# Performance work log

Hardware: AMD Instinct MI355X
Metric: run time of the kernel (lower is better)

Reference implementation:

```python
import math
import jax, jax.numpy as jnp
import numpy as np

N, L, C_IMG, D, FF, H, NL, V = 2, 1024, 512, 512, 2048, 8, 4, 8000
EPS_ATTN = 1e-6
EPS_LN = 1e-5


def pos_enc(position, channels):
    # position: (N, L, 1) float. channels assumed even here (256 / 512).
    num = channels // 2
    log_inc = math.log(10000.0) / (num - 1)
    inv = jnp.exp(jnp.arange(num, dtype=position.dtype) * -log_inc)
    st = position * inv.reshape(1, 1, -1)  # (N, L, num)
    return jnp.concatenate([jnp.sin(st), jnp.cos(st)], -1)


def layer_norm(x, s, b):
    m = jnp.mean(x, -1, keepdims=True)
    v = jnp.mean((x - m) ** 2, -1, keepdims=True)
    return (x - m) / jnp.sqrt(v + EPS_LN) * s + b


def causal_linear_attention(x, mask, Wq, bq, Wk, bk, Wv, bv, Wo, bo):
    # x: (N, L, D), mask: (N, L, 1)
    n, l, d = x.shape
    q = (x @ Wq + bq).reshape(n, l, H, -1)
    k = (x @ Wk + bk).reshape(n, l, H, -1)
    v = (x @ Wv + bv).reshape(n, l, H, -1)
    Q = jax.nn.elu(q) + 1.0                       # elu feature map
    K = (jax.nn.elu(k) + 1.0) * mask[:, :, :, None]
    K_cum = jnp.cumsum(K, axis=1)                 # (N, L, H, dk)
    Z = 1.0 / (jnp.einsum('nlhd,nlhd->nlh', Q, K_cum) + EPS_ATTN)
    KV = jnp.cumsum(K[..., :, None] * v[..., None, :], axis=1)  # (N, L, H, dk, dv)
    out = jnp.einsum('nlhd,nlhde->nlhe', Q, KV) * Z[..., None]
    return out.reshape(n, l, d) @ Wo + bo


def encoder_layer(x, mask, p):
    (Wq, bq, Wk, bk, Wv, bv, Wo, bo, W1, b1, W2, b2, s1, be1, s2, be2) = p
    x = x + causal_linear_attention(x, mask, Wq, bq, Wk, bk, Wv, bv, Wo, bo)
    x = layer_norm(x, s1, be1)
    y = jax.nn.gelu(x @ W1 + b1, approximate=False) @ W2 + b2
    return layer_norm(x + y, s2, be2)


def setup_inputs() -> dict:
    key = jax.random.key(0)
    ks = iter(jax.random.split(key, 64))

    def p(shape):
        return jax.random.normal(next(ks), shape, dtype=jnp.float32) * 0.02

    x_img = jax.random.normal(next(ks), (N, L, C_IMG), dtype=jnp.float32)
    x_txt = jax.random.randint(next(ks), (N, L), 0, V)
    pos = jnp.broadcast_to(jnp.arange(L, dtype=jnp.float32)[None, :, None], (N, L, 1))
    pos_r = jnp.floor(pos / 32.0)
    pos_c = jnp.mod(pos, 32.0)
    pos_t = pos
    first_half = (jnp.arange(L) < L // 2).astype(jnp.float32)[None, :, None]
    mask_img = jnp.broadcast_to(first_half, (N, L, 1))
    mask_txt = 1.0 - mask_img

    inp = dict(x_img=x_img, x_txt=x_txt, mask_img=mask_img, mask_txt=mask_txt,
               pos_r=pos_r, pos_c=pos_c, pos_t=pos_t,
               W_ei=p((C_IMG, D)), b_ei=jnp.zeros((D,)),
               emb_txt=p((V, D)),
               Wq=p((NL, D, D)), bq=jnp.zeros((NL, D)),
               Wk=p((NL, D, D)), bk=jnp.zeros((NL, D)),
               Wv=p((NL, D, D)), bv=jnp.zeros((NL, D)),
               Wo=p((NL, D, D)), bo=jnp.zeros((NL, D)),
               W1=p((NL, D, FF)), b1=jnp.zeros((NL, FF)),
               W2=p((NL, FF, D)), b2=jnp.zeros((NL, D)),
               ln1_s=jnp.ones((NL, D)), ln1_b=jnp.zeros((NL, D)),
               ln2_s=jnp.ones((NL, D)), ln2_b=jnp.zeros((NL, D)),
               W_pi=p((D, C_IMG)), b_pi=jnp.zeros((C_IMG,)),
               W_pt=p((D, V)), b_pt=jnp.zeros((V,)))
    return inp


def reference(x_img, x_txt, mask_img, mask_txt, pos_r, pos_c, pos_t,
              W_ei, b_ei, emb_txt,
              Wq, bq, Wk, bk, Wv, bv, Wo, bo, W1, b1, W2, b2,
              ln1_s, ln1_b, ln2_s, ln2_b, W_pi, b_pi, W_pt, b_pt):
    x_mask = mask_img + mask_txt  # (N, L, 1)
    # image embedding
    half = D // 2
    x_pos = jnp.concatenate([pos_enc(pos_r, half), pos_enc(pos_c, D - half)], -1)
    x_emb_img = ((x_img @ W_ei + b_ei) + x_pos) * mask_img
    # text embedding
    x_emb_txt = (emb_txt[x_txt] + pos_enc(pos_t, D)) * mask_txt
    x = x_emb_img + x_emb_txt
    for i in range(NL):
        p = (Wq[i], bq[i], Wk[i], bk[i], Wv[i], bv[i], Wo[i], bo[i],
             W1[i], b1[i], W2[i], b2[i], ln1_s[i], ln1_b[i], ln2_s[i], ln2_b[i])
        x = encoder_layer(x, x_mask, p)
    logit_img = x @ W_pi + b_pi
    logit_txt = x @ W_pt + b_pt
    return (logit_img, logit_txt)
```

## Files before the change

kernel.cpp:

```cpp
#include <hip/hip_runtime.h>
#include <hip/hip_bf16.h>
#include <math.h>

#define NB 2
#define LSEQ 1024
#define DM 512
#define FFD 2048
#define NHEAD 8
#define DKH 64
#define NLAYER 4
#define VOCAB 8000
#define NCHUNK 16
#define NROWS (NB * LSEQ)
#define QS 1536
#define NHEADCAT 8512
#define NHEADPAD 8576

#define OP_NONE 0
#define OP_GELU 2
#define OP_PART 4
#define OP_HEAD 5

typedef __attribute__((ext_vector_type(8))) short short8;
typedef __attribute__((ext_vector_type(4))) float f32x4;
typedef __hip_bfloat16 bf16;

__device__ __forceinline__ void cast_tile(
    const float* __restrict__ s, bf16* __restrict__ d, int K, int N,
    int n0, int k0, int tid)
{
    __shared__ float tile[32][33];
    const int r  = tid >> 3;
    const int c4 = (tid & 7) * 4;
    const int n  = n0 + c4;
    float4 v = make_float4(0.f, 0.f, 0.f, 0.f);
    if (n < N)
        v = *(const float4*)(s + (size_t)(k0 + r) * N + n);
    tile[r][c4 + 0] = v.x; tile[r][c4 + 1] = v.y;
    tile[r][c4 + 2] = v.z; tile[r][c4 + 3] = v.w;
    __syncthreads();
    const int nr = tid >> 3;
    const int kc = (tid & 7) * 4;
    bf16 o[4];
    o[0] = __float2bfloat16(tile[kc + 0][nr]);
    o[1] = __float2bfloat16(tile[kc + 1][nr]);
    o[2] = __float2bfloat16(tile[kc + 2][nr]);
    o[3] = __float2bfloat16(tile[kc + 3][nr]);
    *(unsigned long long*)(d + (size_t)(n0 + nr) * K + k0 + kc) =
        *(const unsigned long long*)o;
    __syncthreads();
}

#define CO_QKVO 0
#define CO_W1   4096
#define CO_W2   8192
#define CO_WEI  12288
#define CO_WPI  12544
#define CO_WPT  12800
#define CO_XIMG 16832
#define CO_QKVB 17856
#define CO_HB   17860
#define CO_END  17894

__global__ __launch_bounds__(256) void setup_all(
    const float* __restrict__ Wq, const float* __restrict__ Wk,
    const float* __restrict__ Wv, const float* __restrict__ Wo,
    const float* __restrict__ W1, const float* __restrict__ W2,
    const float* __restrict__ Wei, const float* __restrict__ Wpi,
    const float* __restrict__ Wpt,
    bf16* __restrict__ QKVt, bf16* __restrict__ Wot,
    bf16* __restrict__ W1t, bf16* __restrict__ W2t,
    bf16* __restrict__ Weit, bf16* __restrict__ Whead,
    const float* __restrict__ x_img, bf16* __restrict__ ximgh,
    const float* __restrict__ bq, const float* __restrict__ bk,
    const float* __restrict__ bv, float* __restrict__ qkvB,
    const float* __restrict__ bpi, const float* __restrict__ bpt,
    float* __restrict__ hb)
{
    const int id = blockIdx.x;
    const int tid = threadIdx.x;

    if (id < CO_W1) {
        const int rel = id;
        const int z = rel >> 8, t = rel & 255;
        const int layer = z >> 2, which = z & 3;
        const float* src = (which == 0 ? Wq : which == 1 ? Wk : which == 2 ? Wv : Wo)
                           + (size_t)layer * 262144;
        const int n0 = (t & 15) * 32, k0 = (t >> 4) * 32;
        if (which < 3) {
            const int h = n0 >> 6;
            bf16* dst = QKVt + (size_t)layer * 786432
                      + (size_t)(h * 128 + which * 64) * 512;
            cast_tile(src, dst, 512, 512, n0, k0, tid);
        } else {
            cast_tile(src, Wot + (size_t)layer * 262144, 512, 512, n0, k0, tid);
        }
    } else if (id < CO_W2) {
        const int rel = id - CO_W1;
        const int z = rel >> 10, t = rel & 1023;
        cast_tile(W1 + (size_t)z * 1048576, W1t + (size_t)z * 1048576,
                  512, 2048, (t & 63) * 32, (t >> 6) * 32, tid);
    } else if (id < CO_WEI) {
        const int rel = id - CO_W2;
        const int z = rel >> 10, t = rel & 1023;
        cast_tile(W2 + (size_t)z * 1048576, W2t + (size_t)z * 1048576,
                  2048, 512, (t & 15) * 32, (t >> 4) * 32, tid);
    } else if (id < CO_WPI) {
        const int t = id - CO_WEI;
        cast_tile(Wei, Weit, 512, 512, (t & 15) * 32, (t >> 4) * 32, tid);
    } else if (id < CO_WPT) {
        const int t = id - CO_WPI;
        cast_tile(Wpi, Whead, 512, 512, (t & 15) * 32, (t >> 4) * 32, tid);
    } else if (id < CO_XIMG) {
        const int t = id - CO_WPT;
        cast_tile(Wpt, Whead + 262144, 512, VOCAB,
                  (t % 252) * 32, (t / 252) * 32, tid);
    } else if (id < CO_QKVB) {
        const int i = (id - CO_XIMG) * 256 + tid;
        const float4 v = *(const float4*)(x_img + (size_t)i * 4);
        ximgh[(size_t)i * 4 + 0] = __float2bfloat16(v.x);
        ximgh[(size_t)i * 4 + 1] = __float2bfloat16(v.y);
        ximgh[(size_t)i * 4 + 2] = __float2bfloat16(v.z);
        ximgh[(size_t)i * 4 + 3] = __float2bfloat16(v.w);
    } else if (id < CO_HB) {
        const int z = id - CO_QKVB;
        for (int j = tid; j < QS; j += 256) {
            const int h = j / 192, rem = j - h * 192;
            const int which = rem >> 6, idx = rem & 63;
            const float* bsrc = (which == 0 ? bq : which == 1 ? bk : bv);
            qkvB[z * QS + j] = bsrc[z * DM + h * 64 + idx];
        }
    } else {
        const int j = (id - CO_HB) * 256 + tid;
        if (j < NHEADPAD)
            hb[j] = (j < 512) ? bpi[j] : (j < NHEADCAT ? bpt[j - 512] : 0.f);
    }
}

template<int BM, int BN>
__global__ __launch_bounds__(256) void gemm16(
    const bf16* __restrict__ A, const bf16* __restrict__ Bt,
    const float* __restrict__ bias,
    float* __restrict__ outF, float* __restrict__ outF2,
    bf16* __restrict__ outH,
    int M, int K, int Nout, int op, int kslab)
{
    constexpr int WM = BM / 2, WN = BN / 2, MI = WM / 16, NI = WN / 16;
    constexpr int LA = BM / 64, LB = BN / 64;
    constexpr int NL = LA + LB;
    __shared__ bf16 As[2][BM * 32];
    __shared__ bf16 Bs[2][BN * 32];
    const int tid = threadIdx.x;
    const int lane = tid & 63;
    const int wave = tid >> 6;
    const int wm = (wave >> 1) * WM, wn = (wave & 1) * WN;

    int bxi = blockIdx.x, byi = blockIdx.y;
    if (op == OP_HEAD) {
        const int gx = gridDim.x;
        const int nwg = gx * gridDim.y;
        int flat = byi * gx + bxi;
        const int q = nwg >> 3, r = nwg & 7;
        const int xcd = flat & 7, lid = flat >> 3;
        flat = (xcd < r ? xcd * (q + 1) : r * (q + 1) + (xcd - r) * q) + lid;
        bxi = flat % gx;
        byi = flat / gx;
    }
    const int bm = (op == OP_HEAD ? bxi : blockIdx.y) * BM;
    const int bn = (op == OP_HEAD ? byi : blockIdx.x) * BN;
    const int l16 = lane & 15, quad = lane >> 4;

    const int rA = tid >> 2;
    const int c8 = (tid & 3) << 3;

    f32x4 acc[MI][NI];
    #pragma unroll
    for (int i = 0; i < MI; ++i)
        #pragma unroll
        for (int j = 0; j < NI; ++j) acc[i][j] = (f32x4){0.f, 0.f, 0.f, 0.f};

    const bf16* gA = A  + (size_t)(bm + rA) * K + c8;
    const bf16* gB = Bt + (size_t)(bn + rA) * K + c8;
    const int ldsWaveOff = wave * 1024;

    const int kStart = blockIdx.z * kslab;
    const int kEnd = kStart + kslab;

    auto stage = [&](int buf, int k0) {
        #pragma unroll
        for (int i = 0; i < LA; ++i)
            __builtin_amdgcn_global_load_lds(
                (const __attribute__((address_space(1))) void*)(gA + (size_t)i * 64 * K + k0),
                (__attribute__((address_space(3))) void*)((char*)As[buf] + i * 4096 + ldsWaveOff),
                16, 0, 0);
        #pragma unroll
        for (int i = 0; i < LB; ++i)
            __builtin_amdgcn_global_load_lds(
                (const __attribute__((address_space(1))) void*)(gB + (size_t)i * 64 * K + k0),
                (__attribute__((address_space(3))) void*)((char*)Bs[buf] + i * 4096 + ldsWaveOff),
                16, 0, 0);
    };

    stage(0, kStart);
    int cur = 0;
    for (int k0 = kStart; k0 < kEnd; k0 += 32) {
        const bool hasNext = (k0 + 32 < kEnd);
        if (hasNext) {
            stage(cur ^ 1, k0 + 32);
            asm volatile("s_waitcnt vmcnt(%0)" :: "n"(NL) : "memory");
        } else {
            asm volatile("s_waitcnt vmcnt(0)" ::: "memory");
        }
        __builtin_amdgcn_s_barrier();
        short8 a[MI], b[NI];
        #pragma unroll
        for (int i = 0; i < MI; ++i)
            a[i] = *(const short8*)(As[cur] + (size_t)(wm + i * 16 + l16) * 32 + quad * 8);
        #pragma unroll
        for (int j = 0; j < NI; ++j)
            b[j] = *(const short8*)(Bs[cur] + (size_t)(wn + j * 16 + l16) * 32 + quad * 8);
        #pragma unroll
        for (int i = 0; i < MI; ++i)
            #pragma unroll
            for (int j = 0; j < NI; ++j)
                acc[i][j] = __builtin_amdgcn_mfma_f32_16x16x32_bf16(
                    b[j], a[i], acc[i][j], 0, 0, 0);
        __builtin_amdgcn_s_barrier();
        cur ^= 1;
    }

    if (op == OP_PART) {
        float* dst = outF + (size_t)blockIdx.z * (size_t)M * Nout;
        #pragma unroll
        for (int i = 0; i < MI; ++i) {
            const int row = bm + wm + i * 16 + l16;
            #pragma unroll
            for (int j = 0; j < NI; ++j) {
                const int colb = bn + wn + j * 16 + quad * 4;
                *(f32x4*)(dst + (size_t)row * Nout + colb) = acc[i][j];
            }
        }
        return;
    }
    if (op == OP_HEAD) {
        #pragma unroll
        for (int i = 0; i < MI; ++i) {
            const int row = bm + wm + i * 16 + l16;
            #pragma unroll
            for (int j = 0; j < NI; ++j) {
                const int colb = bn + wn + j * 16 + quad * 4;
                const bool cok = (colb < NHEADCAT);
                if (!cok) continue;
                const float4 bz = *(const float4*)(bias + colb);
                f32x4 v = acc[i][j];
                v[0] += bz.x; v[1] += bz.y; v[2] += bz.z; v[3] += bz.w;
                if (colb < 512)
                    *(f32x4*)(outF + (size_t)row * 512 + colb) = v;
                else
                    *(f32x4*)(outF2 + (size_t)row * VOCAB + (colb - 512)) = v;
            }
        }
        return;
    }

    #pragma unroll
    for (int i = 0; i < MI; ++i) {
        const int row = bm + wm + i * 16 + l16;
        #pragma unroll
        for (int j = 0; j < NI; ++j) {
            const int colb = bn + wn + j * 16 + quad * 4;
            if (colb >= Nout) continue;
            const float4 bz = bias ? *(const float4*)(bias + colb)
                                   : make_float4(0.f, 0.f, 0.f, 0.f);
            float v[4];
            #pragma unroll
            for (int r = 0; r < 4; ++r) {
                v[r] = acc[i][j][r] + ((const float*)&bz)[r];
                if (op == OP_GELU)
                    v[r] = 0.5f * v[r] * (1.f + erff(v[r] * 0.70710678118654752f));
            }
            if (outF)
                *(f32x4*)(outF + (size_t)row * Nout + colb) =
                    (f32x4){v[0], v[1], v[2], v[3]};
            if (outH) {
                bf16 o[4];
                o[0] = __float2bfloat16(v[0]); o[1] = __float2bfloat16(v[1]);
                o[2] = __float2bfloat16(v[2]); o[3] = __float2bfloat16(v[3]);
                *(unsigned long long*)(outH + (size_t)row * Nout + colb) =
                    *(const unsigned long long*)o;
            }
        }
    }
}

__global__ __launch_bounds__(256) void qkv_attn(
    const bf16* __restrict__ A, const bf16* __restrict__ Bt,
    const float* __restrict__ bias,
    float* __restrict__ QKVb, float* __restrict__ S, float* __restrict__ ks)
{
    __shared__ char smem[33792];
    const int c = blockIdx.x, h = blockIdx.y, n = blockIdx.z;
    const int tid = threadIdx.x;
    const int lane = tid & 63;
    const int wave = tid >> 6;
    const int l16 = lane & 15, quad = lane >> 4;
    const int r0 = n * LSEQ + c * 64;
    const int wn = wave * 48;

    const bf16* Bh = Bt + (size_t)(h * 192) * 512;
    const float* bh = bias + h * 192;

    f32x4 acc[4][3];
    #pragma unroll
    for (int i = 0; i < 4; ++i)
        #pragma unroll
        for (int j = 0; j < 3; ++j) acc[i][j] = (f32x4){0.f, 0.f, 0.f, 0.f};

    const bf16* gA = A + (size_t)(r0 + (tid >> 2)) * 512 + ((tid & 3) << 3);
    const int ldsWaveOff = wave * 1024;

    auto stage = [&](int buf, int k0) {
        __builtin_amdgcn_global_load_lds(
            (const __attribute__((address_space(1))) void*)(gA + k0),
            (__attribute__((address_space(3))) void*)(smem + buf * 4096 + ldsWaveOff),
            16, 0, 0);
        #pragma unroll
        for (int p = 0; p < 3; ++p)
            __builtin_amdgcn_global_load_lds(
                (const __attribute__((address_space(1))) void*)(
                    Bh + (size_t)(p * 64 + (tid >> 2)) * 512 + ((tid & 3) << 3) + k0),
                (__attribute__((address_space(3))) void*)(
                    smem + 8192 + buf * 12288 + p * 4096 + ldsWaveOff),
                16, 0, 0);
    };

    stage(0, 0);
    int cur = 0;
    for (int k0 = 0; k0 < 512; k0 += 32) {
        if (k0 + 32 < 512) {
            stage(cur ^ 1, k0 + 32);
            asm volatile("s_waitcnt vmcnt(4)" ::: "memory");
        } else {
            asm volatile("s_waitcnt vmcnt(0)" ::: "memory");
        }
        __builtin_amdgcn_s_barrier();
        const bf16* Asb = (const bf16*)(smem + cur * 4096);
        const bf16* Bsb = (const bf16*)(smem + 8192 + cur * 12288);
        short8 a[4], b[3];
        #pragma unroll
        for (int i = 0; i < 4; ++i)
            a[i] = *(const short8*)(Asb + (i * 16 + l16) * 32 + quad * 8);
        #pragma unroll
        for (int j = 0; j < 3; ++j)
            b[j] = *(const short8*)(Bsb + (wn + j * 16 + l16) * 32 + quad * 8);
        #pragma unroll
        for (int i = 0; i < 4; ++i)
            #pragma unroll
            for (int j = 0; j < 3; ++j)
                acc[i][j] = __builtin_amdgcn_mfma_f32_16x16x32_bf16(
                    b[j], a[i], acc[i][j], 0, 0, 0);
        __builtin_amdgcn_s_barrier();
        cur ^= 1;
    }
    __syncthreads();

    float* sK   = (float*)smem;
    float* sV   = (float*)(smem + 16384);
    float* part = (float*)(smem + 32768);

    #pragma unroll
    for (int i = 0; i < 4; ++i) {
        const int row = i * 16 + l16;
        #pragma unroll
        for (int j = 0; j < 3; ++j) {
            const int colb = wn + j * 16 + quad * 4;
            const float4 bz = *(const float4*)(bh + colb);
            float v[4];
            #pragma unroll
            for (int r = 0; r < 4; ++r) {
                v[r] = acc[i][j][r] + ((const float*)&bz)[r];
                if (colb < 128) v[r] = (v[r] > 0.f) ? v[r] + 1.f : expf(v[r]);
            }
            int gcolb;
            if (colb < 64)       gcolb = h * 64 + colb;
            else if (colb < 128) gcolb = 512 + h * 64 + (colb - 64);
            else                 gcolb = 1024 + h * 64 + (colb - 128);
            *(f32x4*)(QKVb + (size_t)(r0 + row) * QS + gcolb) =
                (f32x4){v[0], v[1], v[2], v[3]};
            if (colb >= 128)
                *(f32x4*)(sV + row * 64 + (colb - 128)) = (f32x4){v[0], v[1], v[2], v[3]};
            else if (colb >= 64)
                *(f32x4*)(sK + row * 64 + (colb - 64))  = (f32x4){v[0], v[1], v[2], v[3]};
        }
    }
    __syncthreads();

    const int e = tid & 63, dq = tid >> 6;
    float s[16] = {};
    for (int l = 0; l < 64; ++l) {
        const float vv = sV[l * 64 + e];
        const float4 k0v = *(const float4*)(sK + l * 64 + dq * 16 + 0);
        const float4 k1v = *(const float4*)(sK + l * 64 + dq * 16 + 4);
        const float4 k2v = *(const float4*)(sK + l * 64 + dq * 16 + 8);
        const float4 k3v = *(const float4*)(sK + l * 64 + dq * 16 + 12);
        s[0]  = fmaf(k0v.x, vv, s[0]);  s[1]  = fmaf(k0v.y, vv, s[1]);
        s[2]  = fmaf(k0v.z, vv, s[2]);  s[3]  = fmaf(k0v.w, vv, s[3]);
        s[4]  = fmaf(k1v.x, vv, s[4]);  s[5]  = fmaf(k1v.y, vv, s[5]);
        s[6]  = fmaf(k1v.z, vv, s[6]);  s[7]  = fmaf(k1v.w, vv, s[7]);
        s[8]  = fmaf(k2v.x, vv, s[8]);  s[9]  = fmaf(k2v.y, vv, s[9]);
        s[10] = fmaf(k2v.z, vv, s[10]); s[11] = fmaf(k2v.w, vv, s[11]);
        s[12] = fmaf(k3v.x, vv, s[12]); s[13] = fmaf(k3v.y, vv, s[13]);
        s[14] = fmaf(k3v.z, vv, s[14]); s[15] = fmaf(k3v.w, vv, s[15]);
    }
    const size_t sb = (((size_t)(n * NHEAD + h)) * NCHUNK + c) * 4096;
    #pragma unroll
    for (int i = 0; i < 16; ++i) S[sb + (size_t)(dq * 16 + i) * 64 + e] = s[i];

    float kp = 0.f;
    #pragma unroll
    for (int i = 0; i < 16; ++i) kp += sK[(dq * 16 + i) * 64 + e];
    part[dq * 64 + e] = kp;
    __syncthreads();
    if (tid < 64)
        ks[(((size_t)(n * NHEAD + h)) * NCHUNK + c) * 64 + tid] =
            part[tid] + part[64 + tid] + part[128 + tid] + part[192 + tid];
}

__global__ __launch_bounds__(256) void embed_k(
    const float* __restrict__ gI, const int* __restrict__ xt,
    const float* __restrict__ emb,
    const float* __restrict__ mi, const float* __restrict__ mt,
    const float* __restrict__ pr, const float* __restrict__ pc,
    const float* __restrict__ pt, float* __restrict__ X, bf16* __restrict__ Xh)
{
    const int row = blockIdx.x;
    const float prv = pr[row], pcv = pc[row], ptv = pt[row];
    const float miv = mi[row], mtv = mt[row];
    const int tok = xt[row];
    const float LOG1E4 = 9.2103403719761836f;
    const float LI127 = LOG1E4 / 127.f;
    const float LI255 = LOG1E4 / 255.f;

    for (int d = threadIdx.x; d < DM; d += 256) {
        float ip;
        if (d < 128)       ip = sinf(prv * expf(-(float)d * LI127));
        else if (d < 256)  ip = cosf(prv * expf(-(float)(d - 128) * LI127));
        else if (d < 384)  ip = sinf(pcv * expf(-(float)(d - 256) * LI127));
        else               ip = cosf(pcv * expf(-(float)(d - 384) * LI127));
        float tp;
        if (d < 256) tp = sinf(ptv * expf(-(float)d * LI255));
        else         tp = cosf(ptv * expf(-(float)(d - 256) * LI255));
        const float v = miv * (gI[(size_t)row * DM + d] + ip)
                      + mtv * (emb[(size_t)tok * DM + d] + tp);
        X[(size_t)row * DM + d] = v;
        Xh[(size_t)row * DM + d] = __float2bfloat16(v);
    }
}

__global__ __launch_bounds__(256) void ln_red(
    const float* __restrict__ P, int nP,
    const float* __restrict__ bias, const float* __restrict__ res,
    const float* __restrict__ g, const float* __restrict__ b,
    float* __restrict__ out, bf16* __restrict__ outh)
{
    const int row = blockIdx.x;
    const int tid = threadIdx.x;
    const int lane = tid & 63, wv = tid >> 6;
    const size_t base = (size_t)row * DM;
    float x0 = res[base + tid] + bias[tid];
    float x1 = res[base + tid + 256] + bias[tid + 256];
    for (int p = 0; p < nP; ++p) {
        x0 += P[(size_t)p * 1048576 + base + tid];
        x1 += P[(size_t)p * 1048576 + base + tid + 256];
    }
    __shared__ float redA[4];
    __shared__ float redB[4];
    float s = x0 + x1;
    #pragma unroll
    for (int off = 32; off > 0; off >>= 1) s += __shfl_down(s, off);
    if (lane == 0) redA[wv] = s;
    __syncthreads();
    const float mean = (redA[0] + redA[1] + redA[2] + redA[3]) * (1.f / (float)DM);
    const float d0 = x0 - mean, d1 = x1 - mean;
    float v = d0 * d0 + d1 * d1;
    #pragma unroll
    for (int off = 32; off > 0; off >>= 1) v += __shfl_down(v, off);
    if (lane == 0) redB[wv] = v;
    __syncthreads();
    const float var = (redB[0] + redB[1] + redB[2] + redB[3]) * (1.f / (float)DM);
    const float rstd = rsqrtf(var + 1e-5f);
    const float y0 = d0 * rstd * g[tid] + b[tid];
    const float y1 = d1 * rstd * g[tid + 256] + b[tid + 256];
    out[base + tid]        = y0;
    out[base + tid + 256]  = y1;
    outh[base + tid]       = __float2bfloat16(y0);
    outh[base + tid + 256] = __float2bfloat16(y1);
}

__global__ __launch_bounds__(256) void attn_out(
    const float* __restrict__ QKV, const float* __restrict__ S,
    const float* __restrict__ ks, bf16* __restrict__ O)
{
    const int c = blockIdx.x, h = blockIdx.y, n = blockIdx.z;
    const int tid = threadIdx.x;
    __shared__ float sQt[64][64];
    __shared__ float sKt[64][64];
    __shared__ float sV [64][64];
    __shared__ float sS [64][64];
    __shared__ float sPt[64][65];
    __shared__ float skp[64];

    const size_t nhS = ((size_t)(n * NHEAD + h)) * NCHUNK * 4096;
    const size_t nhK = ((size_t)(n * NHEAD + h)) * NCHUNK * 64;

    {
        float4 aS[4] = {};
        for (int cc = 0; cc < c; ++cc) {
            const float* Sc = S + nhS + (size_t)cc * 4096;
            #pragma unroll
            for (int i = 0; i < 4; ++i) {
                const float4 t = *(const float4*)(Sc + i * 1024 + tid * 4);
                aS[i].x += t.x; aS[i].y += t.y; aS[i].z += t.z; aS[i].w += t.w;
            }
        }
        float* sSf = &sS[0][0];
        #pragma unroll
        for (int i = 0; i < 4; ++i)
            *(float4*)(sSf + i * 1024 + tid * 4) = aS[i];
        if (tid < 64) {
            float kp = 0.f;
            for (int cc = 0; cc < c; ++cc) kp += ks[nhK + cc * 64 + tid];
            skp[tid] = kp;
        }
    }

    const int lr = tid >> 4;
    const int c4 = (tid & 15) * 4;
    #pragma unroll
    for (int it = 0; it < 4; ++it) {
        const int row = it * 16 + lr;
        const size_t gb = ((size_t)(n * LSEQ + c * 64 + row)) * QS + h * DKH + c4;
        const float4 q4 = *(const float4*)(QKV + gb);
        const float4 k4 = *(const float4*)(QKV + gb + 512);
        const float4 v4 = *(const float4*)(QKV + gb + 1024);
        sQt[c4 + 0][row] = q4.x; sQt[c4 + 1][row] = q4.y;
        sQt[c4 + 2][row] = q4.z; sQt[c4 + 3][row] = q4.w;
        sKt[c4 + 0][row] = k4.x; sKt[c4 + 1][row] = k4.y;
        sKt[c4 + 2][row] = k4.z; sKt[c4 + 3][row] = k4.w;
        *(float4*)&sV[row][c4] = v4;
    }
    __syncthreads();

    const int m4 = (tid & 15) * 4;
    const int lg = tid >> 4;
    {
        float p[4][4] = {};
        for (int d = 0; d < 64; ++d) {
            const float4 k4 = *(const float4*)&sKt[d][m4];
            const float4 q4 = *(const float4*)&sQt[d][lg * 4];
            p[0][0] = fmaf(q4.x, k4.x, p[0][0]); p[0][1] = fmaf(q4.x, k4.y, p[0][1]);
            p[0][2] = fmaf(q4.x, k4.z, p[0][2]); p[0][3] = fmaf(q4.x, k4.w, p[0][3]);
            p[1][0] = fmaf(q4.y, k4.x, p[1][0]); p[1][1] = fmaf(q4.y, k4.y, p[1][1]);
            p[1][2] = fmaf(q4.y, k4.z, p[1][2]); p[1][3] = fmaf(q4.y, k4.w, p[1][3]);
            p[2][0] = fmaf(q4.z, k4.x, p[2][0]); p[2][1] = fmaf(q4.z, k4.y, p[2][1]);
            p[2][2] = fmaf(q4.z, k4.z, p[2][2]); p[2][3] = fmaf(q4.z, k4.w, p[2][3]);
            p[3][0] = fmaf(q4.w, k4.x, p[3][0]); p[3][1] = fmaf(q4.w, k4.y, p[3][1]);
            p[3][2] = fmaf(q4.w, k4.z, p[3][2]); p[3][3] = fmaf(q4.w, k4.w, p[3][3]);
        }
        #pragma unroll
        for (int jj = 0; jj < 4; ++jj)
            #pragma unroll
            for (int j = 0; j < 4; ++j)
                sPt[m4 + jj][lg * 4 + j] = p[j][jj];
    }
    __syncthreads();

    float acc[4][4] = {};
    float z[4] = {};
    const int lmax = lg * 4 + 3;
    for (int m = 0; m <= lmax; ++m) {
        const float4 v4 = *(const float4*)&sV[m][m4];
        #pragma unroll
        for (int j = 0; j < 4; ++j) {
            const int l = lg * 4 + j;
            float p = sPt[m][l];
            p = (m <= l) ? p : 0.f;
            z[j] += p;
            acc[j][0] = fmaf(p, v4.x, acc[j][0]);
            acc[j][1] = fmaf(p, v4.y, acc[j][1]);
            acc[j][2] = fmaf(p, v4.z, acc[j][2]);
            acc[j][3] = fmaf(p, v4.w, acc[j][3]);
        }
    }
    for (int d = 0; d < 64; ++d) {
        const float4 s4 = *(const float4*)&sS[d][m4];
        const float4 q4 = *(const float4*)&sQt[d][lg * 4];
        const float kp = skp[d];
        z[0] = fmaf(q4.x, kp, z[0]); z[1] = fmaf(q4.y, kp, z[1]);
        z[2] = fmaf(q4.z, kp, z[2]); z[3] = fmaf(q4.w, kp, z[3]);
        acc[0][0] = fmaf(q4.x, s4.x, acc[0][0]); acc[0][1] = fmaf(q4.x, s4.y, acc[0][1]);
        acc[0][2] = fmaf(q4.x, s4.z, acc[0][2]); acc[0][3] = fmaf(q4.x, s4.w, acc[0][3]);
        acc[1][0] = fmaf(q4.y, s4.x, acc[1][0]); acc[1][1] = fmaf(q4.y, s4.y, acc[1][1]);
        acc[1][2] = fmaf(q4.y, s4.z, acc[1][2]); acc[1][3] = fmaf(q4.y, s4.w, acc[1][3]);
        acc[2][0] = fmaf(q4.z, s4.x, acc[2][0]); acc[2][1] = fmaf(q4.z, s4.y, acc[2][1]);
        acc[2][2] = fmaf(q4.z, s4.z, acc[2][2]); acc[2][3] = fmaf(q4.z, s4.w, acc[2][3]);
        acc[3][0] = fmaf(q4.w, s4.x, acc[3][0]); acc[3][1] = fmaf(q4.w, s4.y, acc[3][1]);
        acc[3][2] = fmaf(q4.w, s4.z, acc[3][2]); acc[3][3] = fmaf(q4.w, s4.w, acc[3][3]);
    }
    #pragma unroll
    for (int j = 0; j < 4; ++j) {
        const int l = lg * 4 + j;
        const float rz = 1.f / (z[j] + 1e-6f);
        const size_t ob = ((size_t)(n * LSEQ + c * 64 + l)) * DM + h * DKH + m4;
        O[ob + 0] = __float2bfloat16(acc[j][0] * rz);
        O[ob + 1] = __float2bfloat16(acc[j][1] * rz);
        O[ob + 2] = __float2bfloat16(acc[j][2] * rz);
        O[ob + 3] = __float2bfloat16(acc[j][3] * rz);
    }
}

extern "C" void kernel_launch(void* const* d_in, const int* in_sizes, int n_in,
                              void* d_out, int out_size, void* d_ws, size_t ws_size,
                              hipStream_t stream)
{
    const float* x_img   = (const float*)d_in[0];
    const int*   x_txt   = (const int*)  d_in[1];
    const float* mask_i  = (const float*)d_in[2];
    const float* mask_t  = (const float*)d_in[3];
    const float* pos_r   = (const float*)d_in[4];
    const float* pos_c   = (const float*)d_in[5];
    const float* pos_t   = (const float*)d_in[6];
    const float* W_ei    = (const float*)d_in[7];
    const float* b_ei    = (const float*)d_in[8];
    const float* emb_txt = (const float*)d_in[9];
    const float* Wq      = (const float*)d_in[10];
    const float* bq      = (const float*)d_in[11];
    const float* Wk      = (const float*)d_in[12];
    const float* bk      = (const float*)d_in[13];
    const float* Wv      = (const float*)d_in[14];
    const float* bv      = (const float*)d_in[15];
    const float* Wo      = (const float*)d_in[16];
    const float* bo      = (const float*)d_in[17];
    const float* W1      = (const float*)d_in[18];
    const float* b1      = (const float*)d_in[19];
    const float* W2      = (const float*)d_in[20];
    const float* b2      = (const float*)d_in[21];
    const float* ln1_s   = (const float*)d_in[22];
    const float* ln1_b   = (const float*)d_in[23];
    const float* ln2_s   = (const float*)d_in[24];
    const float* ln2_b   = (const float*)d_in[25];
    const float* W_pi    = (const float*)d_in[26];
    const float* b_pi    = (const float*)d_in[27];
    const float* W_pt    = (const float*)d_in[28];
    const float* b_pt    = (const float*)d_in[29];

    float* ws = (float*)d_ws;
    size_t off = 0;
    auto alloc = [&](size_t nfloats) { float* p = ws + off; off += nfloats; return p; };

    float* Xb   = alloc(1048576);
    float* Pb   = alloc(4194304);
    float* QKVb = alloc(3145728);
    float* Sb   = alloc(1048576);
    float* ksb  = alloc(16384);
    float* qkvB = alloc(4 * QS);
    float* hb   = alloc(8704);
    bf16* Xh    = (bf16*)alloc(524288);
    bf16* Ob    = (bf16*)alloc(524288);
    bf16* Tb    = (bf16*)alloc(2097152);
    bf16* ximgh = (bf16*)alloc(524288);
    bf16* QKVt  = (bf16*)alloc(1572864);
    bf16* Wot   = (bf16*)alloc(524288);
    bf16* W1t   = (bf16*)alloc(2097152);
    bf16* W2t   = (bf16*)alloc(2097152);
    bf16* Weit  = (bf16*)alloc(131072);
    bf16* Whead = (bf16*)alloc(2195456);

    const dim3 blk(256);
    const dim3 gAttn(NCHUNK, NHEAD, NB);

    setup_all<<<dim3(CO_END), blk, 0, stream>>>(
        Wq, Wk, Wv, Wo, W1, W2, W_ei, W_pi, W_pt,
        QKVt, Wot, W1t, W2t, Weit, Whead,
        x_img, ximgh, bq, bk, bv, qkvB, b_pi, b_pt, hb);

    gemm16<64, 64><<<dim3(8, 32), blk, 0, stream>>>(
        ximgh, Weit, b_ei, Pb, nullptr, nullptr, NROWS, 512, 512, OP_NONE, 512);
    embed_k<<<NROWS, blk, 0, stream>>>(Pb, x_txt, emb_txt, mask_i, mask_t,
                                       pos_r, pos_c, pos_t, Xb, Xh);

    for (int i = 0; i < NLAYER; ++i) {
        qkv_attn<<<gAttn, blk, 0, stream>>>(
            Xh, QKVt + (size_t)i * 786432, qkvB + i * QS, QKVb, Sb, ksb);

        attn_out<<<gAttn, blk, 0, stream>>>(QKVb, Sb, ksb, Ob);

        gemm16<64, 64><<<dim3(8, 32, 2), blk, 0, stream>>>(
            Ob, Wot + (size_t)i * 262144, nullptr,
            Pb, nullptr, nullptr, NROWS, 512, 512, OP_PART, 256);
        ln_red<<<NROWS, blk, 0, stream>>>(Pb, 2, bo + (size_t)i * DM, Xb,
                                          ln1_s + (size_t)i * DM,
                                          ln1_b + (size_t)i * DM, Xb, Xh);

        gemm16<64, 128><<<dim3(16, 32), blk, 0, stream>>>(
            Xh, W1t + (size_t)i * 1048576, b1 + (size_t)i * FFD,
            nullptr, nullptr, Tb, NROWS, 512, FFD, OP_GELU, 512);
        gemm16<64, 64><<<dim3(8, 32, 4), blk, 0, stream>>>(
            Tb, W2t + (size_t)i * 1048576, nullptr,
            Pb, nullptr, nullptr, NROWS, 2048, 512, OP_PART, 512);
        ln_red<<<NROWS, blk, 0, stream>>>(Pb, 4, b2 + (size_t)i * DM, Xb,
                                          ln2_s + (size_t)i * DM,
                                          ln2_b + (size_t)i * DM, Xb, Xh);
    }

    float* out = (float*)d_out;
    gemm16<128, 128><<<dim3(16, 67), blk, 0, stream>>>(
        Xh, Whead, hb, out, out + 1048576, nullptr,
        NROWS, 512, NHEADCAT, OP_HEAD, 512);
}
```

Before: 599.1 us.

## Fuse QKV projection and chunked attention into one cooperative kernel; halve FFN2 split-K

Merges the QKV-projection/chunk-state kernel and the attention-output kernel into a single cooperative kernel that keeps Q, K and V in LDS and uses a grid-wide sync before reading the prefix sums of the chunk states. This removes the fp32 QKV round trip through global memory and one launch per layer. It also cuts the FFN2 split-K factor from 4 to 2, which means fewer partial buffers for ln_red to reduce but less parallelism. The fused kernel uses a lot of LDS (about 100KB), which limits occupancy, and the grid sync relies on all 256 blocks being co-resident.

```diff
diff --git a/kernel.cpp b/kernel.cpp
--- a/kernel.cpp
+++ b/kernel.cpp
@@ -1,6 +1,9 @@
 #include <hip/hip_runtime.h>
 #include <hip/hip_bf16.h>
+#include <hip/hip_cooperative_groups.h>
 #include <math.h>
+
+namespace cg = cooperative_groups;
 
 #define NB 2
 #define LSEQ 1024
@@ -293,12 +296,22 @@
     }
 }
 
-__global__ __launch_bounds__(256) void qkv_attn(
+__global__ __launch_bounds__(256) void attn_fused(
     const bf16* __restrict__ A, const bf16* __restrict__ Bt,
     const float* __restrict__ bias,
-    float* __restrict__ QKVb, float* __restrict__ S, float* __restrict__ ks)
+    float* __restrict__ S, float* __restrict__ ks, bf16* __restrict__ O)
 {
-    __shared__ char smem[33792];
+    __shared__ bf16 As[2][64 * 32];
+    __shared__ bf16 Bs[2][192 * 32];
+    __shared__ float sQt[64][64];
+    __shared__ float sKt[64][64];
+    __shared__ float sV [64][64];
+    __shared__ float sK [64][64];
+    __shared__ float sS [64][64];
+    __shared__ float sPt[64][65];
+    __shared__ float part[4][64];
+    __shared__ float skp[64];
+
     const int c = blockIdx.x, h = blockIdx.y, n = blockIdx.z;
     const int tid = threadIdx.x;
     const int lane = tid & 63;
@@ -322,7 +335,7 @@
     auto stage = [&](int buf, int k0) {
         __builtin_amdgcn_global_load_lds(
             (const __attribute__((address_space(1))) void*)(gA + k0),
-            (__attribute__((address_space(3))) void*)(smem + buf * 4096 + ldsWaveOff),
+            (__attribute__((address_space(3))) void*)((char*)As[buf] + ldsWaveOff),
             16, 0, 0);
         #pragma unroll
         for (int p = 0; p < 3; ++p)
@@ -330,7 +343,7 @@
                 (const __attribute__((address_space(1))) void*)(
                     Bh + (size_t)(p * 64 + (tid >> 2)) * 512 + ((tid & 3) << 3) + k0),
                 (__attribute__((address_space(3))) void*)(
-                    smem + 8192 + buf * 12288 + p * 4096 + ldsWaveOff),
+                    (char*)Bs[buf] + p * 4096 + ldsWaveOff),
                 16, 0, 0);
     };
 
@@ -344,8 +357,8 @@
             asm volatile("s_waitcnt vmcnt(0)" ::: "memory");
         }
         __builtin_amdgcn_s_barrier();
-        const bf16* Asb = (const bf16*)(smem + cur * 4096);
-        const bf16* Bsb = (const bf16*)(smem + 8192 + cur * 12288);
+        const bf16* Asb = As[cur];
+        const bf16* Bsb = Bs[cur];
         short8 a[4], b[3];
         #pragma unroll
         for (int i = 0; i < 4; ++i)
@@ -363,10 +376,6 @@
         cur ^= 1;
     }
     __syncthreads();
-
-    float* sK   = (float*)smem;
-    float* sV   = (float*)(smem + 16384);
-    float* part = (float*)(smem + 32768);
 
     #pragma unroll
     for (int i = 0; i < 4; ++i) {
@@ -381,49 +390,146 @@
                 v[r] = acc[i][j][r] + ((const float*)&bz)[r];
                 if (colb < 128) v[r] = (v[r] > 0.f) ? v[r] + 1.f : expf(v[r]);
             }
-            int gcolb;
-            if (colb < 64)       gcolb = h * 64 + colb;
-            else if (colb < 128) gcolb = 512 + h * 64 + (colb - 64);
-            else                 gcolb = 1024 + h * 64 + (colb - 128);
-            *(f32x4*)(QKVb + (size_t)(r0 + row) * QS + gcolb) =
-                (f32x4){v[0], v[1], v[2], v[3]};
-            if (colb >= 128)
-                *(f32x4*)(sV + row * 64 + (colb - 128)) = (f32x4){v[0], v[1], v[2], v[3]};
-            else if (colb >= 64)
-                *(f32x4*)(sK + row * 64 + (colb - 64))  = (f32x4){v[0], v[1], v[2], v[3]};
+            if (colb < 64) {
+                sQt[colb + 0][row] = v[0]; sQt[colb + 1][row] = v[1];
+                sQt[colb + 2][row] = v[2]; sQt[colb + 3][row] = v[3];
+            } else if (colb < 128) {
+                const int d = colb - 64;
+                sKt[d + 0][row] = v[0]; sKt[d + 1][row] = v[1];
+                sKt[d + 2][row] = v[2]; sKt[d + 3][row] = v[3];
+                *(f32x4*)&sK[row][d] = (f32x4){v[0], v[1], v[2], v[3]};
+            } else {
+                *(f32x4*)&sV[row][colb - 128] = (f32x4){v[0], v[1], v[2], v[3]};
+            }
         }
     }
     __syncthreads();
 
-    const int e = tid & 63, dq = tid >> 6;
-    float s[16] = {};
-    for (int l = 0; l < 64; ++l) {
-        const float vv = sV[l * 64 + e];
-        const float4 k0v = *(const float4*)(sK + l * 64 + dq * 16 + 0);
-        const float4 k1v = *(const float4*)(sK + l * 64 + dq * 16 + 4);
-        const float4 k2v = *(const float4*)(sK + l * 64 + dq * 16 + 8);
-        const float4 k3v = *(const float4*)(sK + l * 64 + dq * 16 + 12);
-        s[0]  = fmaf(k0v.x, vv, s[0]);  s[1]  = fmaf(k0v.y, vv, s[1]);
-        s[2]  = fmaf(k0v.z, vv, s[2]);  s[3]  = fmaf(k0v.w, vv, s[3]);
-        s[4]  = fmaf(k1v.x, vv, s[4]);  s[5]  = fmaf(k1v.y, vv, s[5]);
-        s[6]  = fmaf(k1v.z, vv, s[6]);  s[7]  = fmaf(k1v.w, vv, s[7]);
-        s[8]  = fmaf(k2v.x, vv, s[8]);  s[9]  = fmaf(k2v.y, vv, s[9]);
-        s[10] = fmaf(k2v.z, vv, s[10]); s[11] = fmaf(k2v.w, vv, s[11]);
-        s[12] = fmaf(k3v.x, vv, s[12]); s[13] = fmaf(k3v.y, vv, s[13]);
-        s[14] = fmaf(k3v.z, vv, s[14]); s[15] = fmaf(k3v.w, vv, s[15]);
-    }
-    const size_t sb = (((size_t)(n * NHEAD + h)) * NCHUNK + c) * 4096;
+    {
+        const int e = tid & 63, dq = tid >> 6;
+        float s[16] = {};
+        for (int l = 0; l < 64; ++l) {
+            const float vv = sV[l][e];
+            const float4 k0v = *(const float4*)&sK[l][dq * 16 + 0];
+            const float4 k1v = *(const float4*)&sK[l][dq * 16 + 4];
+            const float4 k2v = *(const float4*)&sK[l][dq * 16 + 8];
+            const float4 k3v = *(const float4*)&sK[l][dq * 16 + 12];
+            s[0]  = fmaf(k0v.x, vv, s[0]);  s[1]  = fmaf(k0v.y, vv, s[1]);
+            s[2]  = fmaf(k0v.z, vv, s[2]);  s[3]  = fmaf(k0v.w, vv, s[3]);
+            s[4]  = fmaf(k1v.x, vv, s[4]);  s[5]  = fmaf(k1v.y, vv, s[5]);
+            s[6]  = fmaf(k1v.z, vv, s[6]);  s[7]  = fmaf(k1v.w, vv, s[7]);
+            s[8]  = fmaf(k2v.x, vv, s[8]);  s[9]  = fmaf(k2v.y, vv, s[9]);
+            s[10] = fmaf(k2v.z, vv, s[10]); s[11] = fmaf(k2v.w, vv, s[11]);
+            s[12] = fmaf(k3v.x, vv, s[12]); s[13] = fmaf(k3v.y, vv, s[13]);
+            s[14] = fmaf(k3v.z, vv, s[14]); s[15] = fmaf(k3v.w, vv, s[15]);
+        }
+        const size_t sb = (((size_t)(n * NHEAD + h)) * NCHUNK + c) * 4096;
+        #pragma unroll
+        for (int i = 0; i < 16; ++i)
+            S[sb + (size_t)(dq * 16 + i) * 64 + e] = s[i];
+
+        float kp = 0.f;
+        #pragma unroll
+        for (int i = 0; i < 16; ++i) kp += sK[dq * 16 + i][e];
+        part[dq][e] = kp;
+        __syncthreads();
+        if (tid < 64)
+            ks[(((size_t)(n * NHEAD + h)) * NCHUNK + c) * 64 + tid] =
+                part[0][tid] + part[1][tid] + part[2][tid] + part[3][tid];
+    }
+
+    cg::this_grid().sync();
+
+    const size_t nhS = ((size_t)(n * NHEAD + h)) * NCHUNK * 4096;
+    const size_t nhK = ((size_t)(n * NHEAD + h)) * NCHUNK * 64;
+    {
+        float4 aS[4] = {};
+        for (int cc = 0; cc < c; ++cc) {
+            const float* Sc = S + nhS + (size_t)cc * 4096;
+            #pragma unroll
+            for (int i = 0; i < 4; ++i) {
+                const float4 t = *(const float4*)(Sc + i * 1024 + tid * 4);
+                aS[i].x += t.x; aS[i].y += t.y; aS[i].z += t.z; aS[i].w += t.w;
+            }
+        }
+        float* sSf = &sS[0][0];
+        #pragma unroll
+        for (int i = 0; i < 4; ++i)
+            *(float4*)(sSf + i * 1024 + tid * 4) = aS[i];
+        if (tid < 64) {
+            float kp = 0.f;
+            for (int cc = 0; cc < c; ++cc) kp += ks[nhK + cc * 64 + tid];
+            skp[tid] = kp;
+        }
+    }
+    __syncthreads();
+
+    const int m4 = (tid & 15) * 4;
+    const int lg = tid >> 4;
+    {
+        float p[4][4] = {};
+        for (int d = 0; d < 64; ++d) {
+            const float4 k4 = *(const float4*)&sKt[d][m4];
+            const float4 q4 = *(const float4*)&sQt[d][lg * 4];
+            p[0][0] = fmaf(q4.x, k4.x, p[0][0]); p[0][1] = fmaf(q4.x, k4.y, p[0][1]);
+            p[0][2] = fmaf(q4.x, k4.z, p[0][2]); p[0][3] = fmaf(q4.x, k4.w, p[0][3]);
+            p[1][0] = fmaf(q4.y, k4.x, p[1][0]); p[1][1] = fmaf(q4.y, k4.y, p[1][1]);
+            p[1][2] = fmaf(q4.y, k4.z, p[1][2]); p[1][3] = fmaf(q4.y, k4.w, p[1][3]);
+            p[2][0] = fmaf(q4.z, k4.x, p[2][0]); p[2][1] = fmaf(q4.z, k4.y, p[2][1]);
+            p[2][2] = fmaf(q4.z, k4.z, p[2][2]); p[2][3] = fmaf(q4.z, k4.w, p[2][3]);
+            p[3][0] = fmaf(q4.w, k4.x, p[3][0]); p[3][1] = fmaf(q4.w, k4.y, p[3][1]);
+            p[3][2] = fmaf(q4.w, k4.z, p[3][2]); p[3][3] = fmaf(q4.w, k4.w, p[3][3]);
+        }
+        #pragma unroll
+        for (int jj = 0; jj < 4; ++jj)
+            #pragma unroll
+            for (int j = 0; j < 4; ++j)
+                sPt[m4 + jj][lg * 4 + j] = p[j][jj];
+    }
+    __syncthreads();
+
+    float acc2[4][4] = {};
+    float z[4] = {};
+    const int lmax = lg * 4 + 3;
+    for (int m = 0; m <= lmax; ++m) {
+        const float4 v4 = *(const float4*)&sV[m][m4];
+        #pragma unroll
+        for (int j = 0; j < 4; ++j) {
+            const int l = lg * 4 + j;
+            float p = sPt[m][l];
+            p = (m <= l) ? p : 0.f;
+            z[j] += p;
+            acc2[j][0] = fmaf(p, v4.x, acc2[j][0]);
+            acc2[j][1] = fmaf(p, v4.y, acc2[j][1]);
+            acc2[j][2] = fmaf(p, v4.z, acc2[j][2]);
+            acc2[j][3] = fmaf(p, v4.w, acc2[j][3]);
+        }
+    }
+    for (int d = 0; d < 64; ++d) {
+        const float4 s4 = *(const float4*)&sS[d][m4];
+        const float4 q4 = *(const float4*)&sQt[d][lg * 4];
+        const float kp = skp[d];
+        z[0] = fmaf(q4.x, kp, z[0]); z[1] = fmaf(q4.y, kp, z[1]);
+        z[2] = fmaf(q4.z, kp, z[2]); z[3] = fmaf(q4.w, kp, z[3]);
+        acc2[0][0] = fmaf(q4.x, s4.x, acc2[0][0]); acc2[0][1] = fmaf(q4.x, s4.y, acc2[0][1]);
+        acc2[0][2] = fmaf(q4.x, s4.z, acc2[0][2]); acc2[0][3] = fmaf(q4.x, s4.w, acc2[0][3]);
+        acc2[1][0] = fmaf(q4.y, s4.x, acc2[1][0]); acc2[1][1] = fmaf(q4.y, s4.y, acc2[1][1]);
+        acc2[1][2] = fmaf(q4.y, s4.z, acc2[1][2]); acc2[1][3] = fmaf(q4.y, s4.w, acc2[1][3]);
+        acc2[2][0] = fmaf(q4.z, s4.x, acc2[2][0]); acc2[2][1] = fmaf(q4.z, s4.y, acc2[2][1]);
+        acc2[2][2] = fmaf(q4.z, s4.z, acc2[2][2]); acc2[2][3] = fmaf(q4.z, s4.w, acc2[2][3]);
+        acc2[3][0] = fmaf(q4.w, s4.x, acc2[3][0]); acc2[3][1] = fmaf(q4.w, s4.y, acc2[3][1]);
+        acc2[3][2] = fmaf(q4.w, s4.z, acc2[3][2]); acc2[3][3] = fmaf(q4.w, s4.w, acc2[3][3]);
+    }
     #pragma unroll
-    for (int i = 0; i < 16; ++i) S[sb + (size_t)(dq * 16 + i) * 64 + e] = s[i];
-
-    float kp = 0.f;
-    #pragma unroll
-    for (int i = 0; i < 16; ++i) kp += sK[(dq * 16 + i) * 64 + e];
-    part[dq * 64 + e] = kp;
-    __syncthreads();
-    if (tid < 64)
-        ks[(((size_t)(n * NHEAD + h)) * NCHUNK + c) * 64 + tid] =
-            part[tid] + part[64 + tid] + part[128 + tid] + part[192 + tid];
+    for (int j = 0; j < 4; ++j) {
+        const int l = lg * 4 + j;
+        const float rz = 1.f / (z[j] + 1e-6f);
+        const size_t ob = ((size_t)(n * LSEQ + c * 64 + l)) * DM + h * DKH + m4;
+        O[ob + 0] = __float2bfloat16(acc2[j][0] * rz);
+        O[ob + 1] = __float2bfloat16(acc2[j][1] * rz);
+        O[ob + 2] = __float2bfloat16(acc2[j][2] * rz);
+        O[ob + 3] = __float2bfloat16(acc2[j][3] * rz);
+    }
 }
 
 __global__ __launch_bounds__(256) void embed_k(
@@ -495,128 +601,6 @@
     out[base + tid + 256]  = y1;
     outh[base + tid]       = __float2bfloat16(y0);
     outh[base + tid + 256] = __float2bfloat16(y1);
-}
-
-__global__ __launch_bounds__(256) void attn_out(
-    const float* __restrict__ QKV, const float* __restrict__ S,
-    const float* __restrict__ ks, bf16* __restrict__ O)
-{
-    const int c = blockIdx.x, h = blockIdx.y, n = blockIdx.z;
-    const int tid = threadIdx.x;
-    __shared__ float sQt[64][64];
-    __shared__ float sKt[64][64];
-    __shared__ float sV [64][64];
-    __shared__ float sS [64][64];
-    __shared__ float sPt[64][65];
-    __shared__ float skp[64];
-
-    const size_t nhS = ((size_t)(n * NHEAD + h)) * NCHUNK * 4096;
-    const size_t nhK = ((size_t)(n * NHEAD + h)) * NCHUNK * 64;
-
-    {
-        float4 aS[4] = {};
-        for (int cc = 0; cc < c; ++cc) {
-            const float* Sc = S + nhS + (size_t)cc * 4096;
-            #pragma unroll
-            for (int i = 0; i < 4; ++i) {
-                const float4 t = *(const float4*)(Sc + i * 1024 + tid * 4);
-                aS[i].x += t.x; aS[i].y += t.y; aS[i].z += t.z; aS[i].w += t.w;
-            }
-        }
-        float* sSf = &sS[0][0];
-        #pragma unroll
-        for (int i = 0; i < 4; ++i)
-            *(float4*)(sSf + i * 1024 + tid * 4) = aS[i];
-        if (tid < 64) {
-            float kp = 0.f;
-            for (int cc = 0; cc < c; ++cc) kp += ks[nhK + cc * 64 + tid];
-            skp[tid] = kp;
-        }
-    }
-
-    const int lr = tid >> 4;
-    const int c4 = (tid & 15) * 4;
-    #pragma unroll
-    for (int it = 0; it < 4; ++it) {
-        const int row = it * 16 + lr;
-        const size_t gb = ((size_t)(n * LSEQ + c * 64 + row)) * QS + h * DKH + c4;
-        const float4 q4 = *(const float4*)(QKV + gb);
-        const float4 k4 = *(const float4*)(QKV + gb + 512);
-        const float4 v4 = *(const float4*)(QKV + gb + 1024);
-        sQt[c4 + 0][row] = q4.x; sQt[c4 + 1][row] = q4.y;
-        sQt[c4 + 2][row] = q4.z; sQt[c4 + 3][row] = q4.w;
-        sKt[c4 + 0][row] = k4.x; sKt[c4 + 1][row] = k4.y;
-        sKt[c4 + 2][row] = k4.z; sKt[c4 + 3][row] = k4.w;
-        *(float4*)&sV[row][c4] = v4;
-    }
-    __syncthreads();
-
-    const int m4 = (tid & 15) * 4;
-    const int lg = tid >> 4;
-    {
-        float p[4][4] = {};
-        for (int d = 0; d < 64; ++d) {
-            const float4 k4 = *(const float4*)&sKt[d][m4];
-            const float4 q4 = *(const float4*)&sQt[d][lg * 4];
-            p[0][0] = fmaf(q4.x, k4.x, p[0][0]); p[0][1] = fmaf(q4.x, k4.y, p[0][1]);
-            p[0][2] = fmaf(q4.x, k4.z, p[0][2]); p[0][3] = fmaf(q4.x, k4.w, p[0][3]);
-            p[1][0] = fmaf(q4.y, k4.x, p[1][0]); p[1][1] = fmaf(q4.y, k4.y, p[1][1]);
-            p[1][2] = fmaf(q4.y, k4.z, p[1][2]); p[1][3] = fmaf(q4.y, k4.w, p[1][3]);
-            p[2][0] = fmaf(q4.z, k4.x, p[2][0]); p[2][1] = fmaf(q4.z, k4.y, p[2][1]);
-            p[2][2] = fmaf(q4.z, k4.z, p[2][2]); p[2][3] = fmaf(q4.z, k4.w, p[2][3]);
-            p[3][0] = fmaf(q4.w, k4.x, p[3][0]); p[3][1] = fmaf(q4.w, k4.y, p[3][1]);
-            p[3][2] = fmaf(q4.w, k4.z, p[3][2]); p[3][3] = fmaf(q4.w, k4.w, p[3][3]);
-        }
-        #pragma unroll
-        for (int jj = 0; jj < 4; ++jj)
-            #pragma unroll
-            for (int j = 0; j < 4; ++j)
-                sPt[m4 + jj][lg * 4 + j] = p[j][jj];
-    }
-    __syncthreads();
-
-    float acc[4][4] = {};
-    float z[4] = {};
-    const int lmax = lg * 4 + 3;
-    for (int m = 0; m <= lmax; ++m) {
-        const float4 v4 = *(const float4*)&sV[m][m4];
-        #pragma unroll
-        for (int j = 0; j < 4; ++j) {
-            const int l = lg * 4 + j;
-            float p = sPt[m][l];
-            p = (m <= l) ? p : 0.f;
-            z[j] += p;
-            acc[j][0] = fmaf(p, v4.x, acc[j][0]);
-            acc[j][1] = fmaf(p, v4.y, acc[j][1]);
-            acc[j][2] = fmaf(p, v4.z, acc[j][2]);
-            acc[j][3] = fmaf(p, v4.w, acc[j][3]);
-        }
-    }
-    for (int d = 0; d < 64; ++d) {
-        const float4 s4 = *(const float4*)&sS[d][m4];
-        const float4 q4 = *(const float4*)&sQt[d][lg * 4];
-        const float kp = skp[d];
-        z[0] = fmaf(q4.x, kp, z[0]); z[1] = fmaf(q4.y, kp, z[1]);
-        z[2] = fmaf(q4.z, kp, z[2]); z[3] = fmaf(q4.w, kp, z[3]);
-        acc[0][0] = fmaf(q4.x, s4.x, acc[0][0]); acc[0][1] = fmaf(q4.x, s4.y, acc[0][1]);
-        acc[0][2] = fmaf(q4.x, s4.z, acc[0][2]); acc[0][3] = fmaf(q4.x, s4.w, acc[0][3]);
-        acc[1][0] = fmaf(q4.y, s4.x, acc[1][0]); acc[1][1] = fmaf(q4.y, s4.y, acc[1][1]);
-        acc[1][2] = fmaf(q4.y, s4.z, acc[1][2]); acc[1][3] = fmaf(q4.y, s4.w, acc[1][3]);
-        acc[2][0] = fmaf(q4.z, s4.x, acc[2][0]); acc[2][1] = fmaf(q4.z, s4.y, acc[2][1]);
-        acc[2][2] = fmaf(q4.z, s4.z, acc[2][2]); acc[2][3] = fmaf(q4.z, s4.w, acc[2][3]);
-        acc[3][0] = fmaf(q4.w, s4.x, acc[3][0]); acc[3][1] = fmaf(q4.w, s4.y, acc[3][1]);
-        acc[3][2] = fmaf(q4.w, s4.z, acc[3][2]); acc[3][3] = fmaf(q4.w, s4.w, acc[3][3]);
-    }
-    #pragma unroll
-    for (int j = 0; j < 4; ++j) {
-        const int l = lg * 4 + j;
-        const float rz = 1.f / (z[j] + 1e-6f);
-        const size_t ob = ((size_t)(n * LSEQ + c * 64 + l)) * DM + h * DKH + m4;
-        O[ob + 0] = __float2bfloat16(acc[j][0] * rz);
-        O[ob + 1] = __float2bfloat16(acc[j][1] * rz);
-        O[ob + 2] = __float2bfloat16(acc[j][2] * rz);
-        O[ob + 3] = __float2bfloat16(acc[j][3] * rz);
-    }
 }
 
 extern "C" void kernel_launch(void* const* d_in, const int* in_sizes, int n_in,
@@ -660,7 +644,6 @@
 
     float* Xb   = alloc(1048576);
     float* Pb   = alloc(4194304);
-    float* QKVb = alloc(3145728);
     float* Sb   = alloc(1048576);
     float* ksb  = alloc(16384);
     float* qkvB = alloc(4 * QS);
@@ -690,10 +673,16 @@
                                        pos_r, pos_c, pos_t, Xb, Xh);
 
     for (int i = 0; i < NLAYER; ++i) {
-        qkv_attn<<<gAttn, blk, 0, stream>>>(
-            Xh, QKVt + (size_t)i * 786432, qkvB + i * QS, QKVb, Sb, ksb);
-
-        attn_out<<<gAttn, blk, 0, stream>>>(QKVb, Sb, ksb, Ob);
+        {
+            const bf16* A_ = Xh;
+            const bf16* B_ = QKVt + (size_t)i * 786432;
+            const float* bias_ = qkvB + i * QS;
+            float* S_ = Sb; float* ks_ = ksb; bf16* O_ = Ob;
+            void* args[] = {(void*)&A_, (void*)&B_, (void*)&bias_,
+                            (void*)&S_, (void*)&ks_, (void*)&O_};
+            hipLaunchCooperativeKernel((void*)attn_fused, gAttn, blk,
+                                       args, 0, stream);
+        }
 
         gemm16<64, 64><<<dim3(8, 32, 2), blk, 0, stream>>>(
             Ob, Wot + (size_t)i * 262144, nullptr,
@@ -705,10 +694,10 @@
         gemm16<64, 128><<<dim3(16, 32), blk, 0, stream>>>(
             Xh, W1t + (size_t)i * 1048576, b1 + (size_t)i * FFD,
             nullptr, nullptr, Tb, NROWS, 512, FFD, OP_GELU, 512);
-        gemm16<64, 64><<<dim3(8, 32, 4), blk, 0, stream>>>(
+        gemm16<64, 64><<<dim3(8, 32, 2), blk, 0, stream>>>(
             Tb, W2t + (size_t)i * 1048576, nullptr,
-            Pb, nullptr, nullptr, NROWS, 2048, 512, OP_PART, 512);
-        ln_red<<<NROWS, blk, 0, stream>>>(Pb, 4, b2 + (size_t)i * DM, Xb,
+            Pb, nullptr, nullptr, NROWS, 2048, 512, OP_PART, 1024);
+        ln_red<<<NROWS, blk, 0, stream>>>(Pb, 2, b2 + (size_t)i * DM, Xb,
                                           ln2_s + (size_t)i * DM,
                                           ln2_b + (size_t)i * DM, Xb, Xh);
     }
```

Measured after the change: 830.2 us. 38.6% more time.
